# Optimization experiments

Measured on AMD Instinct MI355X. Metric: run time of the kernel, lower is better.

Reference implementation:

```python
import jax, jax.numpy as jnp
import numpy as np

N_TOK = 131072
N_EMB = 1024
EMB_DIM = 64
COMMIT = 0.25


def setup_inputs() -> dict:
    key = jax.random.key(0)
    k1, k2 = jax.random.split(key)
    z_e = jax.random.normal(k1, (N_TOK, EMB_DIM), dtype=jnp.float32)
    # nn.init.uniform_(weight, -1/K, 1/K)
    codebook = jax.random.uniform(k2, (N_EMB, EMB_DIM), dtype=jnp.float32,
                                  minval=-1.0 / N_EMB, maxval=1.0 / N_EMB)
    return {"z_e": z_e, "codebook": codebook}


def reference(z_e, codebook):
    sg = jax.lax.stop_gradient
    # ||a-b||^2 = ||a||^2 + ||b||^2 - 2 a.b  (avoids [N,K,D] broadcast)
    d = (jnp.sum(z_e * z_e, axis=-1, keepdims=True)          # [N,1]
         + jnp.sum(codebook * codebook, axis=-1)[None, :]    # [1,K]
         - 2.0 * jnp.einsum('nd,kd->nk', z_e, codebook))     # [N,K]
    indices = jnp.argmin(d, axis=-1)                          # [N] int
    z_q = codebook[indices]                                   # [N,D] gather

    codebook_loss = jnp.mean((z_q - sg(z_e)) ** 2)
    commitment_loss = jnp.mean((z_e - sg(z_q)) ** 2)
    loss = codebook_loss + COMMIT * commitment_loss

    z_q_st = z_e + sg(z_q - z_e)                              # straight-through

    # avg_probs = one_hot(indices).mean(0) via scatter-add histogram
    counts = jnp.zeros((N_EMB,), dtype=jnp.float32).at[indices].add(1.0)
    avg_probs = counts / z_e.shape[0]
    perplexity = jnp.exp(-jnp.sum(avg_probs * jnp.log(avg_probs + 1e-10)))

    return z_q_st, loss, perplexity, indices
```

## Files before the change

kernel.cpp:

```cpp
#include <hip/hip_runtime.h>
#include <math.h>

#define NTOK 131072
#define NEMB 1024
#define DIM  64
#define OUT_LOSS (NTOK * DIM)
#define OUT_PERP (OUT_LOSS + 1)
#define OUT_IDX  (OUT_LOSS + 2)

#define EPS_FLAG 6e-5f

typedef short bf16x8 __attribute__((ext_vector_type(8)));
typedef float f32x4  __attribute__((ext_vector_type(4)));
typedef const __attribute__((address_space(1))) void* gas_t;
typedef __attribute__((address_space(3))) void* las_t;

__device__ __forceinline__ float sqb(float x) {
    float y = x * x;
    asm volatile("" : "+v"(y));
    return y;
}
#define NP_PAIRWISE_SQ64(GET, RES)                                     \
    do {                                                               \
        float r0 = sqb(GET(0)), r1 = sqb(GET(1)), r2 = sqb(GET(2)),    \
              r3 = sqb(GET(3)), r4 = sqb(GET(4)), r5 = sqb(GET(5)),    \
              r6 = sqb(GET(6)), r7 = sqb(GET(7));                      \
        _Pragma("unroll")                                              \
        for (int i = 8; i < 64; i += 8) {                              \
            r0 += sqb(GET(i + 0)); r1 += sqb(GET(i + 1));              \
            r2 += sqb(GET(i + 2)); r3 += sqb(GET(i + 3));              \
            r4 += sqb(GET(i + 4)); r5 += sqb(GET(i + 5));              \
            r6 += sqb(GET(i + 6)); r7 += sqb(GET(i + 7));              \
        }                                                              \
        RES = ((r0 + r1) + (r2 + r3)) + ((r4 + r5) + (r6 + r7));       \
    } while (0)

__device__ __forceinline__ unsigned short f2bf_rne(float x) {
    unsigned u = __float_as_uint(x);
    u += 0x7FFFu + ((u >> 16) & 1u);
    return (unsigned short)(u >> 16);
}
__device__ __forceinline__ float bf2f(unsigned short b) {
    return __uint_as_float(((unsigned)b) << 16);
}


__global__ void vq_prep(const float* __restrict__ cb, float* __restrict__ h,
                        unsigned short* __restrict__ ch, unsigned short* __restrict__ cl,
                        double* __restrict__ sse, int* __restrict__ counts,
                        int* __restrict__ done) {
    if (blockIdx.x == 0) {
        if (threadIdx.x == 0) { *sse = 0.0; *done = 0; }
        for (int i = threadIdx.x; i < NEMB * 16; i += 256) counts[i] = 0;
    }
    int k = blockIdx.x * 256 + threadIdx.x;
    if (k >= NEMB) return;
    float c[64];
    const float4* p = (const float4*)(cb + k * DIM);
#pragma unroll
    for (int q = 0; q < 16; ++q) {
        float4 v = p[q];
        c[4 * q] = v.x; c[4 * q + 1] = v.y; c[4 * q + 2] = v.z; c[4 * q + 3] = v.w;
    }
    float hk;
#define GETC(d) (c[d])
    NP_PAIRWISE_SQ64(GETC, hk);
#undef GETC
    h[k] = hk;
#pragma unroll
    for (int b = 0; b < 8; ++b) {
        unsigned uhv[4], ulv[4];
#pragma unroll
        for (int e = 0; e < 4; ++e) {
            float x0 = -2.0f * c[b * 8 + e * 2 + 0];
            float x1 = -2.0f * c[b * 8 + e * 2 + 1];
            unsigned short h0 = f2bf_rne(x0), h1 = f2bf_rne(x1);
            unsigned short l0 = f2bf_rne(x0 - bf2f(h0)), l1 = f2bf_rne(x1 - bf2f(h1));
            uhv[e] = (unsigned)h0 | ((unsigned)h1 << 16);
            ulv[e] = (unsigned)l0 | ((unsigned)l1 << 16);
        }
        *(uint4*)(ch + k * 64 + b * 8) = make_uint4(uhv[0], uhv[1], uhv[2], uhv[3]);
        *(uint4*)(cl + k * 64 + b * 8) = make_uint4(ulv[0], ulv[1], ulv[2], ulv[3]);
    }
}

__global__ __launch_bounds__(512) void vq_screen(
    const float*          __restrict__ ze,
    const float*          __restrict__ cb,
    const unsigned short* __restrict__ ch_g,
    const unsigned short* __restrict__ cl_g,
    const float*          __restrict__ h_g,
    float*                __restrict__ out,
    double*               __restrict__ sse_g,
    int*                  __restrict__ counts) {
    __shared__ __align__(16) char lds[2 * 16384 + 2 * 256 + 64];
    const int tid  = threadIdx.x;
    const int lane = tid & 63;
    const int wid  = tid >> 6;
    const int col  = lane & 15;
    const int grp  = lane >> 4;
    const int tbase = blockIdx.x * 256 + wid * 32;

    const int srow = tid >> 3, scol = tid & 7;
    const int srcoff = (srow * 8 + (scol ^ (srow & 7))) * 16;

    bf16x8 zh[2][2], zl[2][2];
#pragma unroll
    for (int tt = 0; tt < 2; ++tt)
#pragma unroll
        for (int s = 0; s < 2; ++s) {
            const float* zp = ze + (size_t)(tbase + tt * 16 + col) * 64 + s * 32 + grp * 8;
            float4 v0 = *(const float4*)(zp);
            float4 v1 = *(const float4*)(zp + 4);
            float zv[8] = {v0.x, v0.y, v0.z, v0.w, v1.x, v1.y, v1.z, v1.w};
            bf16x8 hfr, lfr;
#pragma unroll
            for (int j = 0; j < 8; ++j) {
                unsigned short hb = f2bf_rne(zv[j]);
                unsigned short lb = f2bf_rne(zv[j] - bf2f(hb));
                hfr[j] = (short)hb;
                lfr[j] = (short)lb;
            }
            zh[tt][s] = hfr;
            zl[tt][s] = lfr;
        }

    float m1[2] = {INFINITY, INFINITY}, m2[2] = {INFINITY, INFINITY};
    int   ki[2] = {0, 0};

#define STAGE(cc, b)                                                           \
    do {                                                                       \
        __builtin_amdgcn_global_load_lds(                                      \
            (gas_t)((const char*)ch_g + (cc) * 8192 + srcoff),                 \
            (las_t)(lds + (b) * 16384 + wid * 1024), 16, 0, 0);                \
        __builtin_amdgcn_global_load_lds(                                      \
            (gas_t)((const char*)cl_g + (cc) * 8192 + srcoff),                 \
            (las_t)(lds + (b) * 16384 + 8192 + wid * 1024), 16, 0, 0);         \
        if (wid == 0)                                                          \
            __builtin_amdgcn_global_load_lds(                                  \
                (gas_t)(h_g + (cc) * 64 + lane),                               \
                (las_t)(lds + 32768 + (b) * 256), 4, 0, 0);                    \
    } while (0)

    STAGE(0, 0);
    __syncthreads();

    for (int cc = 0; cc < 16; ++cc) {
        int b = cc & 1;
        if (cc + 1 < 16) STAGE(cc + 1, b ^ 1);

        for (int ct = 0; ct < 4; ++ct) {
            const int arow = b * 16384 + ct * 2048 + col * 128;
            bf16x8 ach0 = *(const bf16x8*)(lds + arow + ((((0 * 4) + grp) ^ (col & 7)) << 4));
            bf16x8 ach1 = *(const bf16x8*)(lds + arow + ((((1 * 4) + grp) ^ (col & 7)) << 4));
            bf16x8 acl0 = *(const bf16x8*)(lds + arow + 8192 + ((((0 * 4) + grp) ^ (col & 7)) << 4));
            bf16x8 acl1 = *(const bf16x8*)(lds + arow + 8192 + ((((1 * 4) + grp) ^ (col & 7)) << 4));
            f32x4 hv = *(const f32x4*)(lds + 32768 + b * 256 + ct * 64 + grp * 16);

            f32x4 acc0 = hv, acc1 = hv;
            acc0 = __builtin_amdgcn_mfma_f32_16x16x32_bf16(ach0, zh[0][0], acc0, 0, 0, 0);
            acc1 = __builtin_amdgcn_mfma_f32_16x16x32_bf16(ach0, zh[1][0], acc1, 0, 0, 0);
            acc0 = __builtin_amdgcn_mfma_f32_16x16x32_bf16(ach1, zh[0][1], acc0, 0, 0, 0);
            acc1 = __builtin_amdgcn_mfma_f32_16x16x32_bf16(ach1, zh[1][1], acc1, 0, 0, 0);
            acc0 = __builtin_amdgcn_mfma_f32_16x16x32_bf16(ach0, zl[0][0], acc0, 0, 0, 0);
            acc1 = __builtin_amdgcn_mfma_f32_16x16x32_bf16(ach0, zl[1][0], acc1, 0, 0, 0);
            acc0 = __builtin_amdgcn_mfma_f32_16x16x32_bf16(ach1, zl[0][1], acc0, 0, 0, 0);
            acc1 = __builtin_amdgcn_mfma_f32_16x16x32_bf16(ach1, zl[1][1], acc1, 0, 0, 0);
            acc0 = __builtin_amdgcn_mfma_f32_16x16x32_bf16(acl0, zh[0][0], acc0, 0, 0, 0);
            acc1 = __builtin_amdgcn_mfma_f32_16x16x32_bf16(acl0, zh[1][0], acc1, 0, 0, 0);
            acc0 = __builtin_amdgcn_mfma_f32_16x16x32_bf16(acl1, zh[0][1], acc0, 0, 0, 0);
            acc1 = __builtin_amdgcn_mfma_f32_16x16x32_bf16(acl1, zh[1][1], acc1, 0, 0, 0);

            const int kb = cc * 64 + ct * 16 + grp * 4;
#pragma unroll
            for (int j = 0; j < 4; ++j) {
                float s0 = acc0[j], s1 = acc1[j];
                bool lt0 = s0 < m1[0], lt1 = s1 < m1[1];
                m2[0] = fminf(m2[0], fmaxf(s0, m1[0]));
                m2[1] = fminf(m2[1], fmaxf(s1, m1[1]));
                ki[0] = lt0 ? (kb + j) : ki[0];
                ki[1] = lt1 ? (kb + j) : ki[1];
                m1[0] = fminf(m1[0], s0);
                m1[1] = fminf(m1[1], s1);
            }
        }
        __syncthreads();
    }

#pragma unroll
    for (int d = 16; d <= 32; d <<= 1) {
#pragma unroll
        for (int tt = 0; tt < 2; ++tt) {
            float om1 = __shfl_xor(m1[tt], d, 64);
            float om2 = __shfl_xor(m2[tt], d, 64);
            int   oki = __shfl_xor(ki[tt], d, 64);
            m2[tt] = fminf(fminf(m2[tt], om2), fmaxf(m1[tt], om1));
            ki[tt] = (om1 < m1[tt]) ? oki : ki[tt];
            m1[tt] = fminf(m1[tt], om1);
        }
    }
    unsigned flagpack = ((m2[0] - m1[0] < EPS_FLAG) ? 1u : 0u)
                      | ((m2[1] - m1[1] < EPS_FLAG) ? 2u : 0u);
    if (lane < 16) {
#pragma unroll
        for (int tt = 0; tt < 2; ++tt) {
            int t = tbase + tt * 16 + lane;
            bool flag = (flagpack >> tt) & 1u;
            out[OUT_IDX + t] = flag ? -(float)(ki[tt] + 1) : (float)ki[tt];
        }
    }

    double lsse = 0.0;
    const int d4 = lane & 15;
#pragma unroll
    for (int iter = 0; iter < 8; ++iter) {
        const int j   = iter * 4 + grp;
        const int tt  = iter >> 2;
        const int src = j & 15;
        int k = __shfl(ki[tt], src, 64);
        unsigned fp = __shfl(flagpack, src, 64);
        if (!((fp >> tt) & 1u)) {
            const int t = tbase + j;
            float4 q  = *(const float4*)(cb + k * DIM + d4 * 4);
            float4 zv = *(const float4*)(ze + (size_t)t * DIM + d4 * 4);
            *(float4*)(out + (size_t)t * DIM + d4 * 4) = q;
            double dx = (double)q.x - (double)zv.x;
            double dy = (double)q.y - (double)zv.y;
            double dz = (double)q.z - (double)zv.z;
            double dw = (double)q.w - (double)zv.w;
            lsse = fma(dx, dx, lsse); lsse = fma(dy, dy, lsse);
            lsse = fma(dz, dz, lsse); lsse = fma(dw, dw, lsse);
            if (d4 == 0) atomicAdd(&counts[k * 16], 1);
        }
    }
#pragma unroll
    for (int off = 32; off > 0; off >>= 1)
        lsse += __shfl_down(lsse, off, 64);
    double* red = (double*)(lds + 33280);
    if (lane == 0) red[wid] = lsse;
    __syncthreads();
    if (tid == 0) {
        double bs = ((red[0] + red[1]) + (red[2] + red[3]))
                  + ((red[4] + red[5]) + (red[6] + red[7]));
        atomicAdd(sse_g, bs);
    }
}

__global__ __launch_bounds__(512) void vq_rescue(
    const float* __restrict__ ze, const float* __restrict__ cb,
    const float* __restrict__ h_g, float* __restrict__ out,
    double* __restrict__ sse_g, int* __restrict__ counts,
    int* __restrict__ done) {
    __shared__ __align__(16) float4 cbl[512 * 17];
    __shared__ float zst[8][64];
    __shared__ unsigned long long keys[8][64];
    __shared__ float hl[NEMB];
    __shared__ int loc[512];
    __shared__ int nloc;
    __shared__ double red[8];
    __shared__ int flagS;
    const int tid  = threadIdx.x;
    const int lane = tid & 63;
    const int wid  = tid >> 6;
    const int tbase = blockIdx.x * 512;

    if (tid == 0) nloc = 0;
    for (int i = tid; i < NEMB; i += 512) hl[i] = h_g[i];
    __syncthreads();
    float fidx = out[OUT_IDX + tbase + tid];
    if (fidx < 0.0f) { int s = atomicAdd(&nloc, 1); loc[s] = tid; }
    __syncthreads();
    const int nq = nloc;
    double lsse = 0.0;

    if (nq > 0) {
        const float4* cb4 = (const float4*)cb;
        for (int hf = 0; hf < 2; ++hf) {
            __syncthreads();
#pragma unroll
            for (int j = 0; j < 16; ++j) {
                int f = tid + j * 512;
                int code = f >> 4, d4 = f & 15;
                cbl[code * 17 + d4] = cb4[(size_t)(hf * 512 + code) * 16 + d4];
            }
            __syncthreads();

            for (int i = wid; i < nq; i += 8) {
                const int t = tbase + loc[i];
                const int slot = i >> 3;

                zst[wid][lane] = ze[(size_t)t * 64 + lane];
                __builtin_amdgcn_wave_barrier();
                asm volatile("s_waitcnt lgkmcnt(0)" ::: "memory");
                __builtin_amdgcn_sched_barrier(0);

                float sz;
#define GZ(d) (zst[wid][d])
                NP_PAIRWISE_SQ64(GZ, sz);
#undef GZ

                float acc[8] = {0.f, 0.f, 0.f, 0.f, 0.f, 0.f, 0.f, 0.f};
                const float4* zr4 = (const float4*)zst[wid];
#pragma unroll
                for (int d4 = 0; d4 < 16; ++d4) {
                    float4 zq = zr4[d4];
#pragma unroll
                    for (int cc = 0; cc < 8; ++cc) {
                        float4 cv = cbl[(lane + 64 * cc) * 17 + d4];
                        acc[cc] = fmaf(cv.x, zq.x, acc[cc]);
                        acc[cc] = fmaf(cv.y, zq.y, acc[cc]);
                        acc[cc] = fmaf(cv.z, zq.z, acc[cc]);
                        acc[cc] = fmaf(cv.w, zq.w, acc[cc]);
                    }
                }
                unsigned long long key = ~0ull;
#pragma unroll
                for (int cc = 0; cc < 8; ++cc) {
                    unsigned k = (unsigned)(hf * 512 + lane + 64 * cc);
                    float dk = (sz + hl[k]) - 2.0f * acc[cc];
                    unsigned long long c =
                        ((unsigned long long)__float_as_uint(dk) << 32) | k;
                    key = c < key ? c : key;
                }
#pragma unroll
                for (int dd = 1; dd < 64; dd <<= 1) {
                    unsigned long long o = __shfl_xor(key, dd, 64);
                    key = o < key ? o : key;
                }
                if (hf == 0) {
                    if (lane == 0) keys[wid][slot] = key;
                } else {
                    unsigned long long k0 = keys[wid][slot];
                    if (k0 < key) key = k0;
                    int newk = (int)(unsigned)(key & 0xFFFFFFFFull);
                    float q  = cb[newk * 64 + lane];
                    float zv = zst[wid][lane];
                    out[(size_t)t * 64 + lane] = q;
                    double diff = (double)q - (double)zv;
                    lsse = fma(diff, diff, lsse);
                    if (lane == 0) {
                        out[OUT_IDX + t] = (float)newk;
                        atomicAdd(&counts[newk * 16], 1);
                    }
                }
            }
        }
    }

#pragma unroll
    for (int off = 32; off > 0; off >>= 1)
        lsse += __shfl_down(lsse, off, 64);
    if (lane == 0) red[wid] = lsse;
    __syncthreads();
    if (tid == 0) {
        double bs = ((red[0] + red[1]) + (red[2] + red[3]))
                  + ((red[4] + red[5]) + (red[6] + red[7]));
        if (bs != 0.0) atomicAdd(sse_g, bs);
        __threadfence();
        flagS = (atomicAdd(done, 1) == 255);
    }
    __syncthreads();

    if (flagS) {
        __threadfence();
        double* red2 = (double*)cbl;
        double local = 0.0;
        for (int k = tid; k < NEMB; k += 512) {
            int cv = __hip_atomic_load(&counts[k * 16], __ATOMIC_RELAXED, __HIP_MEMORY_SCOPE_AGENT);
            double p = (double)cv / (double)NTOK;
            local += p * log(p + 1e-10);
        }
        red2[tid] = local;
        __syncthreads();
        for (int s = 256; s > 0; s >>= 1) {
            if (tid < s) red2[tid] += red2[tid + s];
            __syncthreads();
        }
        if (tid == 0) {
            double sv = __hip_atomic_load(sse_g, __ATOMIC_RELAXED, __HIP_MEMORY_SCOPE_AGENT);
            double mse = sv / ((double)NTOK * (double)DIM);
            out[OUT_LOSS] = (float)(1.25 * mse);
            out[OUT_PERP] = (float)exp(-red2[0]);
        }
    }
}

extern "C" void kernel_launch(void* const* d_in, const int* in_sizes, int n_in,
                              void* d_out, int out_size, void* d_ws, size_t ws_size,
                              hipStream_t stream) {
    const float* ze = (const float*)d_in[0];
    const float* cb = (const float*)d_in[1];
    float* out = (float*)d_out;

    char* w = (char*)d_ws;
    double*         sse    = (double*)w;
    int*            counts = (int*)(w + 64);
    int*            done   = (int*)(w + 65600);
    float*          h      = (float*)(w + 65664);
    unsigned short* ch     = (unsigned short*)(w + 69760);
    unsigned short* cl     = (unsigned short*)(w + 200832);

    vq_prep<<<NEMB / 256, 256, 0, stream>>>(cb, h, ch, cl, sse, counts, done);
    vq_screen<<<NTOK / 256, 512, 0, stream>>>(ze, cb, ch, cl, h, out, sse, counts);
    vq_rescue<<<NTOK / 512, 512, 0, stream>>>(ze, cb, h, out, sse, counts, done);
}
```

Before: 126.2 us.

## Triple-buffer codebook staging with explicit vmcnt waits and unrolled chunk loop

Replaces the double-buffered codebook staging loop with a three-buffer pipeline. Each chunk now waits only on its own global-to-LDS loads through explicit s_waitcnt vmcnt counts before one barrier, so the prefetch two chunks ahead stays in flight during compute. Previously the end-of-loop syncthreads could force the just-issued prefetch to drain. The codebook norm vector is loaded into LDS once up front instead of per chunk, and the 16-chunk loop is fully unrolled. LDS use per block rises to about 53 KB, which may lower the number of resident blocks.

```diff
diff --git a/kernel.cpp b/kernel.cpp
--- a/kernel.cpp
+++ b/kernel.cpp
@@ -93,7 +93,7 @@
     float*                __restrict__ out,
     double*               __restrict__ sse_g,
     int*                  __restrict__ counts) {
-    __shared__ __align__(16) char lds[2 * 16384 + 2 * 256 + 64];
+    __shared__ __align__(16) char lds[53376];
     const int tid  = threadIdx.x;
     const int lane = tid & 63;
     const int wid  = tid >> 6;
@@ -136,56 +136,66 @@
         __builtin_amdgcn_global_load_lds(                                      \
             (gas_t)((const char*)cl_g + (cc) * 8192 + srcoff),                 \
             (las_t)(lds + (b) * 16384 + 8192 + wid * 1024), 16, 0, 0);         \
-        if (wid == 0)                                                          \
-            __builtin_amdgcn_global_load_lds(                                  \
-                (gas_t)(h_g + (cc) * 64 + lane),                               \
-                (las_t)(lds + 32768 + (b) * 256), 4, 0, 0);                    \
     } while (0)
 
+#define COMPUTE(cc, b)                                                         \
+    do {                                                                       \
+        _Pragma("unroll")                                                      \
+        for (int ct = 0; ct < 4; ++ct) {                                       \
+            const int arow = (b) * 16384 + ct * 2048 + col * 128;              \
+            bf16x8 ach0 = *(const bf16x8*)(lds + arow + ((((0 * 4) + grp) ^ (col & 7)) << 4)); \
+            bf16x8 ach1 = *(const bf16x8*)(lds + arow + ((((1 * 4) + grp) ^ (col & 7)) << 4)); \
+            bf16x8 acl0 = *(const bf16x8*)(lds + arow + 8192 + ((((0 * 4) + grp) ^ (col & 7)) << 4)); \
+            bf16x8 acl1 = *(const bf16x8*)(lds + arow + 8192 + ((((1 * 4) + grp) ^ (col & 7)) << 4)); \
+            f32x4 hv = *(const f32x4*)(lds + 49152 + (cc) * 256 + ct * 64 + grp * 16); \
+            f32x4 acc0 = hv, acc1 = hv;                                        \
+            acc0 = __builtin_amdgcn_mfma_f32_16x16x32_bf16(ach0, zh[0][0], acc0, 0, 0, 0); \
+            acc1 = __builtin_amdgcn_mfma_f32_16x16x32_bf16(ach0, zh[1][0], acc1, 0, 0, 0); \
+            acc0 = __builtin_amdgcn_mfma_f32_16x16x32_bf16(ach1, zh[0][1], acc0, 0, 0, 0); \
+            acc1 = __builtin_amdgcn_mfma_f32_16x16x32_bf16(ach1, zh[1][1], acc1, 0, 0, 0); \
+            acc0 = __builtin_amdgcn_mfma_f32_16x16x32_bf16(ach0, zl[0][0], acc0, 0, 0, 0); \
+            acc1 = __builtin_amdgcn_mfma_f32_16x16x32_bf16(ach0, zl[1][0], acc1, 0, 0, 0); \
+            acc0 = __builtin_amdgcn_mfma_f32_16x16x32_bf16(ach1, zl[0][1], acc0, 0, 0, 0); \
+            acc1 = __builtin_amdgcn_mfma_f32_16x16x32_bf16(ach1, zl[1][1], acc1, 0, 0, 0); \
+            acc0 = __builtin_amdgcn_mfma_f32_16x16x32_bf16(acl0, zh[0][0], acc0, 0, 0, 0); \
+            acc1 = __builtin_amdgcn_mfma_f32_16x16x32_bf16(acl0, zh[1][0], acc1, 0, 0, 0); \
+            acc0 = __builtin_amdgcn_mfma_f32_16x16x32_bf16(acl1, zh[0][1], acc0, 0, 0, 0); \
+            acc1 = __builtin_amdgcn_mfma_f32_16x16x32_bf16(acl1, zh[1][1], acc1, 0, 0, 0); \
+            const int kb = (cc) * 64 + ct * 16 + grp * 4;                      \
+            _Pragma("unroll")                                                  \
+            for (int j = 0; j < 4; ++j) {                                      \
+                float s0 = acc0[j], s1 = acc1[j];                              \
+                bool lt0 = s0 < m1[0], lt1 = s1 < m1[1];                       \
+                m2[0] = fminf(m2[0], fmaxf(s0, m1[0]));                        \
+                m2[1] = fminf(m2[1], fmaxf(s1, m1[1]));                        \
+                ki[0] = lt0 ? (kb + j) : ki[0];                                \
+                ki[1] = lt1 ? (kb + j) : ki[1];                                \
+                m1[0] = fminf(m1[0], s0);                                      \
+                m1[1] = fminf(m1[1], s1);                                      \
+            }                                                                  \
+        }                                                                      \
+    } while (0)
+
+#define CHUNK(cc, W)                                                           \
+    do {                                                                       \
+        asm volatile("s_waitcnt vmcnt(" #W ")" ::: "memory");                  \
+        __builtin_amdgcn_s_barrier();                                          \
+        __builtin_amdgcn_sched_barrier(0);                                     \
+        if ((cc) + 2 < 16) STAGE((cc) + 2, ((cc) + 2) % 3);                    \
+        COMPUTE(cc, (cc) % 3);                                                 \
+    } while (0)
+
+    __builtin_amdgcn_global_load_lds((gas_t)(h_g + tid),
+                                     (las_t)(lds + 49152 + wid * 256), 4, 0, 0);
+    __builtin_amdgcn_global_load_lds((gas_t)(h_g + 512 + tid),
+                                     (las_t)(lds + 49152 + 2048 + wid * 256), 4, 0, 0);
     STAGE(0, 0);
-    __syncthreads();
-
-    for (int cc = 0; cc < 16; ++cc) {
-        int b = cc & 1;
-        if (cc + 1 < 16) STAGE(cc + 1, b ^ 1);
-
-        for (int ct = 0; ct < 4; ++ct) {
-            const int arow = b * 16384 + ct * 2048 + col * 128;
-            bf16x8 ach0 = *(const bf16x8*)(lds + arow + ((((0 * 4) + grp) ^ (col & 7)) << 4));
-            bf16x8 ach1 = *(const bf16x8*)(lds + arow + ((((1 * 4) + grp) ^ (col & 7)) << 4));
-            bf16x8 acl0 = *(const bf16x8*)(lds + arow + 8192 + ((((0 * 4) + grp) ^ (col & 7)) << 4));
-            bf16x8 acl1 = *(const bf16x8*)(lds + arow + 8192 + ((((1 * 4) + grp) ^ (col & 7)) << 4));
-            f32x4 hv = *(const f32x4*)(lds + 32768 + b * 256 + ct * 64 + grp * 16);
-
-            f32x4 acc0 = hv, acc1 = hv;
-            acc0 = __builtin_amdgcn_mfma_f32_16x16x32_bf16(ach0, zh[0][0], acc0, 0, 0, 0);
-            acc1 = __builtin_amdgcn_mfma_f32_16x16x32_bf16(ach0, zh[1][0], acc1, 0, 0, 0);
-            acc0 = __builtin_amdgcn_mfma_f32_16x16x32_bf16(ach1, zh[0][1], acc0, 0, 0, 0);
-            acc1 = __builtin_amdgcn_mfma_f32_16x16x32_bf16(ach1, zh[1][1], acc1, 0, 0, 0);
-            acc0 = __builtin_amdgcn_mfma_f32_16x16x32_bf16(ach0, zl[0][0], acc0, 0, 0, 0);
-            acc1 = __builtin_amdgcn_mfma_f32_16x16x32_bf16(ach0, zl[1][0], acc1, 0, 0, 0);
-            acc0 = __builtin_amdgcn_mfma_f32_16x16x32_bf16(ach1, zl[0][1], acc0, 0, 0, 0);
-            acc1 = __builtin_amdgcn_mfma_f32_16x16x32_bf16(ach1, zl[1][1], acc1, 0, 0, 0);
-            acc0 = __builtin_amdgcn_mfma_f32_16x16x32_bf16(acl0, zh[0][0], acc0, 0, 0, 0);
-            acc1 = __builtin_amdgcn_mfma_f32_16x16x32_bf16(acl0, zh[1][0], acc1, 0, 0, 0);
-            acc0 = __builtin_amdgcn_mfma_f32_16x16x32_bf16(acl1, zh[0][1], acc0, 0, 0, 0);
-            acc1 = __builtin_amdgcn_mfma_f32_16x16x32_bf16(acl1, zh[1][1], acc1, 0, 0, 0);
-
-            const int kb = cc * 64 + ct * 16 + grp * 4;
-#pragma unroll
-            for (int j = 0; j < 4; ++j) {
-                float s0 = acc0[j], s1 = acc1[j];
-                bool lt0 = s0 < m1[0], lt1 = s1 < m1[1];
-                m2[0] = fminf(m2[0], fmaxf(s0, m1[0]));
-                m2[1] = fminf(m2[1], fmaxf(s1, m1[1]));
-                ki[0] = lt0 ? (kb + j) : ki[0];
-                ki[1] = lt1 ? (kb + j) : ki[1];
-                m1[0] = fminf(m1[0], s0);
-                m1[1] = fminf(m1[1], s1);
-            }
-        }
-        __syncthreads();
-    }
+    STAGE(1, 1);
+
+    CHUNK(0, 2);  CHUNK(1, 2);  CHUNK(2, 2);  CHUNK(3, 2);
+    CHUNK(4, 2);  CHUNK(5, 2);  CHUNK(6, 2);  CHUNK(7, 2);
+    CHUNK(8, 2);  CHUNK(9, 2);  CHUNK(10, 2); CHUNK(11, 2);
+    CHUNK(12, 2); CHUNK(13, 2); CHUNK(14, 2); CHUNK(15, 0);
 
 #pragma unroll
     for (int d = 16; d <= 32; d <<= 1) {
@@ -236,7 +246,7 @@
 #pragma unroll
     for (int off = 32; off > 0; off >>= 1)
         lsse += __shfl_down(lsse, off, 64);
-    double* red = (double*)(lds + 33280);
+    double* red = (double*)(lds + 53312);
     if (lane == 0) red[wid] = lsse;
     __syncthreads();
     if (tid == 0) {
```

Result: no change. 125.6 us (-0.5%).
